# Optimization experiments

Measured on AMD Instinct MI355X. Metric: run time of the kernel, lower is better.

Reference implementation:

```python
import jax, jax.numpy as jnp
import numpy as np

B, S, D = 2, 4096, 768
H = 12
HD = D // H  # 64
INNER = 4 * D
EPS = 1e-5


def setup_inputs() -> dict:
    key = jax.random.key(0)
    ks = jax.random.split(key, 12)
    sd = 0.02
    # causal additive mask (GPT-2 style): 0 where allowed, -1e9 where masked
    causal = jnp.tril(jnp.ones((S, S), dtype=bool))
    attention_mask = jnp.where(causal, 0.0, -1e9).astype(jnp.float32)[None, None]
    return {
        "hidden_states": jax.random.normal(ks[0], (B, S, D), dtype=jnp.float32),
        "attention_mask": attention_mask,
        "ln1_g": jnp.ones((D,), jnp.float32),
        "ln1_b": jnp.zeros((D,), jnp.float32),
        "w_attn": jax.random.normal(ks[1], (D, 3 * D), jnp.float32) * sd,
        "b_attn": jnp.zeros((3 * D,), jnp.float32),
        "w_cproj": jax.random.normal(ks[2], (D, D), jnp.float32) * sd,
        "b_cproj": jnp.zeros((D,), jnp.float32),
        "ln2_g": jnp.ones((D,), jnp.float32),
        "ln2_b": jnp.zeros((D,), jnp.float32),
        "w_fc": jax.random.normal(ks[3], (D, INNER), jnp.float32) * sd,
        "b_fc": jnp.zeros((INNER,), jnp.float32),
        "w_fc_proj": jax.random.normal(ks[4], (INNER, D), jnp.float32) * sd,
        "b_fc_proj": jnp.zeros((D,), jnp.float32),
    }


def _layernorm(x, g, b):
    mu = jnp.mean(x, axis=-1, keepdims=True)
    var = jnp.mean(jnp.square(x - mu), axis=-1, keepdims=True)
    return (x - mu) * jax.lax.rsqrt(var + EPS) * g + b


def reference(hidden_states, attention_mask, ln1_g, ln1_b, w_attn, b_attn,
              w_cproj, b_cproj, ln2_g, ln2_b, w_fc, b_fc, w_fc_proj, b_fc_proj):
    residual = hidden_states
    x = _layernorm(hidden_states, ln1_g, ln1_b)
    # qkv projection
    qkv = x @ w_attn + b_attn                       # [B,S,3D]
    q, k, v = jnp.split(qkv, 3, axis=-1)
    q = q.reshape(B, S, H, HD).transpose(0, 2, 1, 3)  # [B,H,S,HD]
    k = k.reshape(B, S, H, HD).transpose(0, 2, 1, 3)
    v = v.reshape(B, S, H, HD).transpose(0, 2, 1, 3)
    scale = HD ** -0.5
    scores = jnp.einsum('bhqd,bhkd->bhqk', q, k) * scale + attention_mask
    attn = jax.nn.softmax(scores, axis=-1)
    ctx = jnp.einsum('bhqk,bhkd->bhqd', attn, v)    # [B,H,S,HD]
    ctx = ctx.transpose(0, 2, 1, 3).reshape(B, S, D)
    attn_out = ctx @ w_cproj + b_cproj
    h = attn_out + residual
    residual = h
    y = _layernorm(h, ln2_g, ln2_b)
    y = jax.nn.gelu(y @ w_fc + b_fc, approximate=False)  # nn.GELU default = exact
    y = y @ w_fc_proj + b_fc_proj
    return y + residual
```

## Files before the change

kernel.cpp:

```cpp
#include <hip/hip_runtime.h>
#include <hip/hip_bf16.h>


#define S_     4096
#define D_     768
#define H_     12
#define HD_    64
#define NB_    2
#define M_     (NB_*S_)
#define QKV_   (3*D_)
#define INNER_ 3072

typedef unsigned short u16;
typedef __attribute__((ext_vector_type(4))) float f32x4;
typedef __attribute__((ext_vector_type(8))) short s16x8;

__device__ __forceinline__ float bf2f(u16 h) {
    union { unsigned int u; float f; } c; c.u = ((unsigned int)h) << 16; return c.f;
}
__device__ __forceinline__ u16 f2bf(float f) {
    union { float f; unsigned int u; } c; c.f = f;
    return (u16)((c.u + 0x7fffu + ((c.u >> 16) & 1u)) >> 16);
}
__device__ __forceinline__ void storev(u16* p, float v) { *p = f2bf(v); }
__device__ __forceinline__ void storev(float* p, float v) { *p = v; }

__device__ __forceinline__ float fexp2(float x) {
#if __has_builtin(__builtin_amdgcn_exp2f)
    return __builtin_amdgcn_exp2f(x);
#else
    return __expf(x * 0.69314718056f);
#endif
}
__device__ __forceinline__ unsigned int packbf(float a, float b) {
    union { __hip_bfloat162 h; unsigned int u; } c;
    c.h = __float22bfloat162_rn(float2{a, b});
    return c.u;
}

__device__ __forceinline__ void gload_lds16(const u16* g, u16* l) {
    __builtin_amdgcn_global_load_lds((const __attribute__((address_space(1))) void*)g,
                                     (__attribute__((address_space(3))) void*)l, 16, 0, 0);
}

template <typename IT, bool PERM>
__global__ __launch_bounds__(256) void transpose_kernel(const IT* __restrict__ in,
                                                        u16* __restrict__ out,
                                                        int ld_in, int ld_out) {
    __shared__ u16 tile[32][33];
    const int c0 = blockIdx.x * 32, r0 = blockIdx.y * 32;
    const int tx = threadIdx.x & 31, ty = threadIdx.x >> 5;
#pragma unroll
    for (int i = 0; i < 32; i += 8) {
        IT v = in[(size_t)(r0 + ty + i) * ld_in + c0 + tx];
        u16 bv;
        if constexpr (sizeof(IT) == 4) bv = f2bf((float)v); else bv = (u16)v;
        tile[ty + i][tx] = bv;
    }
    __syncthreads();
    int oc = r0 + tx;
    if constexpr (PERM) oc = (oc & ~63) | (((oc & 15) << 2) | ((oc >> 4) & 3));
#pragma unroll
    for (int i = 0; i < 32; i += 8)
        out[(size_t)(c0 + ty + i) * ld_out + oc] = tile[tx][ty + i];
}

__global__ __launch_bounds__(256) void ln_row(const float* __restrict__ x, const float* __restrict__ g,
                                              const float* __restrict__ bb, u16* __restrict__ y) {
    const int row = blockIdx.x;
    const int tid = threadIdx.x;
    const float* xr = x + (size_t)row * D_;
    float v0 = xr[tid], v1 = xr[tid + 256], v2 = xr[tid + 512];
    float s = v0 + v1 + v2, s2 = v0 * v0 + v1 * v1 + v2 * v2;
#pragma unroll
    for (int d = 32; d >= 1; d >>= 1) { s += __shfl_xor(s, d, 64); s2 += __shfl_xor(s2, d, 64); }
    __shared__ float red[8];
    const int wave = tid >> 6, lane = tid & 63;
    if (lane == 0) { red[wave] = s; red[4 + wave] = s2; }
    __syncthreads();
    s = red[0] + red[1] + red[2] + red[3];
    s2 = red[4] + red[5] + red[6] + red[7];
    const float mu = s * (1.0f / D_);
    const float var = s2 * (1.0f / D_) - mu * mu;
    const float rstd = rsqrtf(var + 1e-5f);
    u16* yr = y + (size_t)row * D_;
    yr[tid]       = f2bf((v0 - mu) * rstd * g[tid]       + bb[tid]);
    yr[tid + 256] = f2bf((v1 - mu) * rstd * g[tid + 256] + bb[tid + 256]);
    yr[tid + 512] = f2bf((v2 - mu) * rstd * g[tid + 512] + bb[tid + 512]);
}

template <int EPI, typename OT>
__global__ __launch_bounds__(256) void gemm_bt(const u16* __restrict__ A, const u16* __restrict__ Bt,
                                               const float* __restrict__ bias, const float* res,
                                               OT* C, int M, int N, int K) {
    __shared__ u16 As[128 * 32];
    __shared__ u16 Bs[128 * 32];
    const int tid = threadIdx.x;
    const int wave = tid >> 6, lane = tid & 63;
    const int m0 = blockIdx.y << 7, n0 = blockIdx.x << 7;
    const int fr = lane & 15, quad = lane >> 4;

    const int srow = wave * 16 + (lane >> 2);
    const int scol = (lane & 3) * 8;
    const u16* ag0 = A + (size_t)(m0 + srow) * K + scol;
    const u16* ag1 = ag0 + (size_t)64 * K;
    const u16* bg0 = Bt + (size_t)(n0 + srow) * K + scol;
    const u16* bg1 = bg0 + (size_t)64 * K;
    u16* al0 = As + wave * 512;
    u16* al1 = As + 2048 + wave * 512;
    u16* bl0 = Bs + wave * 512;
    u16* bl1 = Bs + 2048 + wave * 512;

    const f32x4 fz = {0.f, 0.f, 0.f, 0.f};
    f32x4 acc[4][4];
#pragma unroll
    for (int i = 0; i < 4; i++)
#pragma unroll
        for (int j = 0; j < 4; j++) acc[i][j] = fz;

    const int wm = wave & 1, wn = wave >> 1;
    const u16* a_rd = As + (wm * 64 + fr) * 32 + quad * 8;
    const u16* b_rd = Bs + (wn * 64 + fr) * 32 + quad * 8;

    for (int k0 = 0; k0 < K; k0 += 32) {
        gload_lds16(ag0 + k0, al0);
        gload_lds16(ag1 + k0, al1);
        gload_lds16(bg0 + k0, bl0);
        gload_lds16(bg1 + k0, bl1);
        __syncthreads();
        s16x8 af[4], bfr[4];
#pragma unroll
        for (int t = 0; t < 4; t++) {
            af[t]  = *(const s16x8*)(a_rd + t * 16 * 32);
            bfr[t] = *(const s16x8*)(b_rd + t * 16 * 32);
        }
#pragma unroll
        for (int mt = 0; mt < 4; mt++)
#pragma unroll
            for (int nt = 0; nt < 4; nt++)
                acc[mt][nt] = __builtin_amdgcn_mfma_f32_16x16x32_bf16(af[mt], bfr[nt], acc[mt][nt], 0, 0, 0);
        __syncthreads();
    }

    const int crow0 = m0 + wm * 64 + quad * 4;
    const int ccol0 = n0 + wn * 64 + fr;
#pragma unroll
    for (int nt = 0; nt < 4; nt++) {
        const int col = ccol0 + nt * 16;
        const float bv = bias[col];
#pragma unroll
        for (int mt = 0; mt < 4; mt++) {
#pragma unroll
            for (int r = 0; r < 4; r++) {
                const int row = crow0 + mt * 16 + r;
                float v = acc[mt][nt][r] + bv;
                if constexpr (EPI == 1) v = 0.5f * v * (1.0f + erff(v * 0.70710678118654752f));
                if constexpr (EPI == 2) v += res[(size_t)row * N + col];
                storev(&C[(size_t)row * N + col], v);
            }
        }
    }
}

template <int EPI, typename OT>
__global__ __launch_bounds__(256) void gemm_bt64(const u16* __restrict__ A, const u16* __restrict__ Bt,
                                                 const float* __restrict__ bias, const float* res,
                                                 OT* C, int M, int N, int K) {
    __shared__ u16 As[128 * 32];
    __shared__ u16 Bs[64 * 32];
    const int tid = threadIdx.x;
    const int wave = tid >> 6, lane = tid & 63;
    const int m0 = blockIdx.y << 7, n0 = blockIdx.x << 6;
    const int fr = lane & 15, quad = lane >> 4;

    const int srow = wave * 16 + (lane >> 2);
    const int scol = (lane & 3) * 8;
    const u16* ag0 = A + (size_t)(m0 + srow) * K + scol;
    const u16* ag1 = ag0 + (size_t)64 * K;
    const u16* bg0 = Bt + (size_t)(n0 + srow) * K + scol;
    u16* al0 = As + wave * 512;
    u16* al1 = As + 2048 + wave * 512;
    u16* bl0 = Bs + wave * 512;

    const f32x4 fz = {0.f, 0.f, 0.f, 0.f};
    f32x4 acc[2][4];
#pragma unroll
    for (int i = 0; i < 2; i++)
#pragma unroll
        for (int j = 0; j < 4; j++) acc[i][j] = fz;

    const u16* a_rd = As + (wave * 32 + fr) * 32 + quad * 8;
    const u16* b_rd = Bs + fr * 32 + quad * 8;

    for (int k0 = 0; k0 < K; k0 += 32) {
        gload_lds16(ag0 + k0, al0);
        gload_lds16(ag1 + k0, al1);
        gload_lds16(bg0 + k0, bl0);
        __syncthreads();
        s16x8 af[2], bfr[4];
#pragma unroll
        for (int t = 0; t < 2; t++) af[t] = *(const s16x8*)(a_rd + t * 16 * 32);
#pragma unroll
        for (int t = 0; t < 4; t++) bfr[t] = *(const s16x8*)(b_rd + t * 16 * 32);
#pragma unroll
        for (int mt = 0; mt < 2; mt++)
#pragma unroll
            for (int nt = 0; nt < 4; nt++)
                acc[mt][nt] = __builtin_amdgcn_mfma_f32_16x16x32_bf16(af[mt], bfr[nt], acc[mt][nt], 0, 0, 0);
        __syncthreads();
    }

    const int crow0 = m0 + wave * 32 + quad * 4;
    const int ccol0 = n0 + fr;
#pragma unroll
    for (int nt = 0; nt < 4; nt++) {
        const int col = ccol0 + nt * 16;
        const float bv = bias[col];
#pragma unroll
        for (int mt = 0; mt < 2; mt++) {
#pragma unroll
            for (int r = 0; r < 4; r++) {
                const int row = crow0 + mt * 16 + r;
                float v = acc[mt][nt][r] + bv;
                if constexpr (EPI == 1) v = 0.5f * v * (1.0f + erff(v * 0.70710678118654752f));
                if constexpr (EPI == 2) v += res[(size_t)row * N + col];
                storev(&C[(size_t)row * N + col], v);
            }
        }
    }
}

#define SCALE_ 0.1803368801111f
#define PST_ 72
__global__ __launch_bounds__(256, 2) void flash_attn(const u16* __restrict__ qkv, const u16* __restrict__ vt,
                                                     u16* __restrict__ ctx) {
    const int strip = (int)(gridDim.x - 1 - blockIdx.x);
    const int h = blockIdx.y, b = blockIdx.z;
    const int tid = threadIdx.x;
    const int wave = tid >> 6, lane = tid & 63;
    const int fr = lane & 15, quad = lane >> 4;
    const int q0 = strip << 7;
    const int qwv = q0 + (wave << 5);

    __shared__ u16 Ks[2][64 * 64];
    __shared__ u16 Vs[2][64 * 64];
    __shared__ u16 Ps4[4][32 * PST_];
    u16* Ps = Ps4[wave];

    const u16* Qg  = qkv + ((size_t)b * S_ + qwv) * QKV_ + h * HD_;
    const u16* Kg  = qkv + (size_t)b * S_ * QKV_ + D_ + h * HD_;
    const u16* Vtg = vt + ((size_t)b * D_ + h * HD_) * S_;

    const int rsub = lane >> 3;
    const int schunk = ((lane & 7) ^ rsub) << 3;
    const u16* KgS = Kg + (size_t)((wave << 4) + rsub) * QKV_ + schunk;
    const u16* VgS = Vtg + (size_t)((wave << 4) + rsub) * S_ + schunk;
    u16* KlS0 = &Ks[0][(wave << 4) * 64];
    u16* VlS0 = &Vs[0][(wave << 4) * 64];

    s16x8 qf[2][2];
#pragma unroll
    for (int mt = 0; mt < 2; mt++)
#pragma unroll
        for (int kk = 0; kk < 2; kk++)
            qf[mt][kk] = *(const s16x8*)(Qg + (size_t)(mt * 16 + fr) * QKV_ + kk * 32 + quad * 8);

    const f32x4 fz = {0.f, 0.f, 0.f, 0.f};
    f32x4 o[2][4];
    f32x4 ls[2];
#pragma unroll
    for (int mt = 0; mt < 2; mt++) {
        ls[mt] = fz;
#pragma unroll
        for (int nt = 0; nt < 4; nt++) o[mt][nt] = fz;
    }
    s16x8 ones;
#pragma unroll
    for (int j = 0; j < 8; j++) ones[j] = (short)0x3F80;

    const int ntw = (strip << 1) + 2;

    {
        const u16* kg = KgS;
        const u16* vg = VgS;
        gload_lds16(kg, KlS0);
        gload_lds16(kg + (size_t)8 * QKV_, KlS0 + 512);
        gload_lds16(vg, VlS0);
        gload_lds16(vg + (size_t)8 * S_, VlS0 + 512);
    }
    asm volatile("s_waitcnt vmcnt(0)" ::: "memory");
    __syncthreads();

    int cur = 0;
    for (int t = 0; t < ntw; t++) {
        const int k0 = t << 6;

        if (t + 1 < ntw) {
            const int nb = cur ^ 1;
            const u16* kg = KgS + (size_t)((t + 1) << 6) * QKV_;
            const u16* vg = VgS + ((t + 1) << 6);
            u16* kl = KlS0 + nb * (64 * 64);
            u16* vl = VlS0 + nb * (64 * 64);
            gload_lds16(kg, kl);
            gload_lds16(kg + (size_t)8 * QKV_, kl + 512);
            gload_lds16(vg, vl);
            gload_lds16(vg + (size_t)8 * S_, vl + 512);
        }

        if (k0 <= qwv + 31) {
            const u16* kb = Ks[cur];
            const u16* vb = Vs[cur];

            s16x8 kc[2][4];
#pragma unroll
            for (int kk = 0; kk < 2; kk++)
#pragma unroll
                for (int nt = 0; nt < 4; nt++) {
                    const int row = nt * 16 + fr;
                    const int sl = ((kk * 4 + quad) ^ (fr & 7)) << 3;
                    kc[kk][nt] = *(const s16x8*)(kb + row * 64 + sl);
                }

            f32x4 sc[2][4];
#pragma unroll
            for (int mt = 0; mt < 2; mt++)
#pragma unroll
                for (int nt = 0; nt < 4; nt++) sc[mt][nt] = fz;
#pragma unroll
            for (int kk = 0; kk < 2; kk++)
#pragma unroll
                for (int mt = 0; mt < 2; mt++)
#pragma unroll
                    for (int nt = 0; nt < 4; nt++)
                        sc[mt][nt] = __builtin_amdgcn_mfma_f32_16x16x32_bf16(qf[mt][kk], kc[kk][nt], sc[mt][nt], 0, 0, 0);

            const bool fast = (k0 + 63 <= qwv);
#pragma unroll
            for (int mt = 0; mt < 2; mt++) {
#pragma unroll
                for (int r = 0; r < 4; r++) {
                    float s0 = sc[mt][0][r] * SCALE_;
                    float s1 = sc[mt][1][r] * SCALE_;
                    float s2 = sc[mt][2][r] * SCALE_;
                    float s3 = sc[mt][3][r] * SCALE_;
                    if (!fast) {
                        const int lim = (qwv + mt * 16 + quad * 4 + r) - k0;
                        if (fr      > lim) s0 = -1e30f;
                        if (fr + 16 > lim) s1 = -1e30f;
                        if (fr + 32 > lim) s2 = -1e30f;
                        if (fr + 48 > lim) s3 = -1e30f;
                    }
                    s0 = fexp2(s0); s1 = fexp2(s1); s2 = fexp2(s2); s3 = fexp2(s3);
                    const int prow = mt * 16 + quad * 4 + r;
                    *(uint2*)(Ps + prow * PST_ + fr * 4) = make_uint2(packbf(s0, s1), packbf(s2, s3));
                }
            }

            s16x8 vf[2][4];
#pragma unroll
            for (int kk = 0; kk < 2; kk++)
#pragma unroll
                for (int nt = 0; nt < 4; nt++) {
                    const int row = nt * 16 + fr;
                    const int sl = ((kk * 4 + quad) ^ (fr & 7)) << 3;
                    vf[kk][nt] = *(const s16x8*)(vb + row * 64 + sl);
                }

            s16x8 pf[2][2];
#pragma unroll
            for (int mt = 0; mt < 2; mt++)
#pragma unroll
                for (int kk = 0; kk < 2; kk++)
                    pf[mt][kk] = *(const s16x8*)(Ps + (mt * 16 + fr) * PST_ + kk * 32 + quad * 8);

#pragma unroll
            for (int mt = 0; mt < 2; mt++) {
                ls[mt] = __builtin_amdgcn_mfma_f32_16x16x32_bf16(pf[mt][0], ones, ls[mt], 0, 0, 0);
                ls[mt] = __builtin_amdgcn_mfma_f32_16x16x32_bf16(pf[mt][1], ones, ls[mt], 0, 0, 0);
            }
#pragma unroll
            for (int kk = 0; kk < 2; kk++)
#pragma unroll
                for (int mt = 0; mt < 2; mt++)
#pragma unroll
                    for (int nt = 0; nt < 4; nt++)
                        o[mt][nt] = __builtin_amdgcn_mfma_f32_16x16x32_bf16(pf[mt][kk], vf[kk][nt], o[mt][nt], 0, 0, 0);
        }

        asm volatile("s_waitcnt vmcnt(0)" ::: "memory");
        __syncthreads();
        cur ^= 1;
    }

#pragma unroll
    for (int mt = 0; mt < 2; mt++) {
#pragma unroll
        for (int r = 0; r < 4; r++) {
            const int grow = qwv + mt * 16 + quad * 4 + r;
            const float inv = 1.0f / ls[mt][r];
            u16* crow = ctx + ((size_t)b * S_ + grow) * D_ + h * HD_ + fr;
#pragma unroll
            for (int nt = 0; nt < 4; nt++)
                crow[nt * 16] = f2bf(o[mt][nt][r] * inv);
        }
    }
}

extern "C" void kernel_launch(void* const* d_in, const int* in_sizes, int n_in,
                              void* d_out, int out_size, void* d_ws, size_t ws_size,
                              hipStream_t stream) {
    const float* hid    = (const float*)d_in[0];
    const float* ln1g   = (const float*)d_in[2];
    const float* ln1b   = (const float*)d_in[3];
    const float* w_attn = (const float*)d_in[4];
    const float* b_attn = (const float*)d_in[5];
    const float* w_cp   = (const float*)d_in[6];
    const float* b_cp   = (const float*)d_in[7];
    const float* ln2g   = (const float*)d_in[8];
    const float* ln2b   = (const float*)d_in[9];
    const float* w_fc   = (const float*)d_in[10];
    const float* b_fc   = (const float*)d_in[11];
    const float* w_fp   = (const float*)d_in[12];
    const float* b_fp   = (const float*)d_in[13];
    float* dout = (float*)d_out;

    u16* ws = (u16*)d_ws;
    u16* wTa  = ws; ws += (size_t)QKV_ * D_;
    u16* wTc  = ws; ws += (size_t)D_ * D_;
    u16* wTf  = ws; ws += (size_t)INNER_ * D_;
    u16* wTp  = ws; ws += (size_t)D_ * INNER_;
    u16* xln  = ws; ws += (size_t)M_ * D_;
    u16* qkvb = ws; ws += (size_t)M_ * QKV_;
    u16* vtb  = ws; ws += (size_t)NB_ * D_ * S_;
    u16* ctxb = xln;
    u16* yln  = xln;
    u16* act  = qkvb;

    dim3 blk(256);
    transpose_kernel<float, false><<<dim3(QKV_ / 32, D_ / 32), blk, 0, stream>>>(w_attn, wTa, QKV_, D_);
    transpose_kernel<float, false><<<dim3(D_ / 32, D_ / 32), blk, 0, stream>>>(w_cp, wTc, D_, D_);
    transpose_kernel<float, false><<<dim3(INNER_ / 32, D_ / 32), blk, 0, stream>>>(w_fc, wTf, INNER_, D_);
    transpose_kernel<float, false><<<dim3(D_ / 32, INNER_ / 32), blk, 0, stream>>>(w_fp, wTp, D_, INNER_);

    ln_row<<<M_, blk, 0, stream>>>(hid, ln1g, ln1b, xln);
    gemm_bt<0, u16><<<dim3(QKV_ / 128, M_ / 128), blk, 0, stream>>>(xln, wTa, b_attn, nullptr, qkvb, M_, QKV_, D_);

    transpose_kernel<u16, true><<<dim3(D_ / 32, S_ / 32), blk, 0, stream>>>(qkvb + 2 * D_, vtb, QKV_, S_);
    transpose_kernel<u16, true><<<dim3(D_ / 32, S_ / 32), blk, 0, stream>>>(qkvb + (size_t)S_ * QKV_ + 2 * D_,
                                                                            vtb + (size_t)D_ * S_, QKV_, S_);
    flash_attn<<<dim3(S_ / 128, H_, NB_), dim3(256), 0, stream>>>(qkvb, vtb, ctxb);

    gemm_bt64<2, float><<<dim3(D_ / 64, M_ / 128), blk, 0, stream>>>(ctxb, wTc, b_cp, hid, dout, M_, D_, D_);
    ln_row<<<M_, blk, 0, stream>>>(dout, ln2g, ln2b, yln);
    gemm_bt<1, u16><<<dim3(INNER_ / 128, M_ / 128), blk, 0, stream>>>(yln, wTf, b_fc, nullptr, act, M_, INNER_, D_);
    gemm_bt64<2, float><<<dim3(D_ / 64, M_ / 128), blk, 0, stream>>>(act, wTp, b_fp, dout, dout, M_, D_, INNER_);
}
```

Measured before the change: 545.2 us.

## Use persistent flash-attention blocks with atomic work queue, longest strips first

Replaces the fixed 3D grid for flash attention with 512 persistent blocks that fetch work items through an atomic counter. Items are ordered longest causal strip first so that load balancing across CUs improves and the tail is reduced. The counter lives in the output buffer and is zeroed by the first layernorm kernel; the output is overwritten later. This adds an atomic and a barrier per item, plus reliance on the output buffer as scratch.

Measured after the change: 527.9 us. 1.03x faster.

```diff
diff --git a/kernel.cpp b/kernel.cpp
--- a/kernel.cpp
+++ b/kernel.cpp
@@ -66,9 +66,11 @@
 }
 
 __global__ __launch_bounds__(256) void ln_row(const float* __restrict__ x, const float* __restrict__ g,
-                                              const float* __restrict__ bb, u16* __restrict__ y) {
+                                              const float* __restrict__ bb, u16* __restrict__ y,
+                                              unsigned int* ctr) {
     const int row = blockIdx.x;
     const int tid = threadIdx.x;
+    if (ctr && row == 0 && tid == 0) *ctr = 0u;
     const float* xr = x + (size_t)row * D_;
     float v0 = xr[tid], v1 = xr[tid + 256], v2 = xr[tid + 512];
     float s = v0 + v1 + v2, s2 = v0 * v0 + v1 * v1 + v2 * v2;
@@ -230,178 +232,187 @@
     }
 }
 
-#define SCALE_ 0.1803368801111f
-#define PST_ 72
+#define SCALE_  0.1803368801111f
+#define PST_    72
+#define NITEMS_ (32 * H_ * NB_)
+#define NWORK_  512
 __global__ __launch_bounds__(256, 2) void flash_attn(const u16* __restrict__ qkv, const u16* __restrict__ vt,
-                                                     u16* __restrict__ ctx) {
-    const int strip = (int)(gridDim.x - 1 - blockIdx.x);
-    const int h = blockIdx.y, b = blockIdx.z;
+                                                     u16* __restrict__ ctx, unsigned int* __restrict__ ctr) {
     const int tid = threadIdx.x;
     const int wave = tid >> 6, lane = tid & 63;
     const int fr = lane & 15, quad = lane >> 4;
-    const int q0 = strip << 7;
-    const int qwv = q0 + (wave << 5);
 
     __shared__ u16 Ks[2][64 * 64];
     __shared__ u16 Vs[2][64 * 64];
     __shared__ u16 Ps4[4][32 * PST_];
+    __shared__ int item_sh;
     u16* Ps = Ps4[wave];
-
-    const u16* Qg  = qkv + ((size_t)b * S_ + qwv) * QKV_ + h * HD_;
-    const u16* Kg  = qkv + (size_t)b * S_ * QKV_ + D_ + h * HD_;
-    const u16* Vtg = vt + ((size_t)b * D_ + h * HD_) * S_;
 
     const int rsub = lane >> 3;
     const int schunk = ((lane & 7) ^ rsub) << 3;
-    const u16* KgS = Kg + (size_t)((wave << 4) + rsub) * QKV_ + schunk;
-    const u16* VgS = Vtg + (size_t)((wave << 4) + rsub) * S_ + schunk;
     u16* KlS0 = &Ks[0][(wave << 4) * 64];
     u16* VlS0 = &Vs[0][(wave << 4) * 64];
 
-    s16x8 qf[2][2];
-#pragma unroll
-    for (int mt = 0; mt < 2; mt++)
-#pragma unroll
-        for (int kk = 0; kk < 2; kk++)
-            qf[mt][kk] = *(const s16x8*)(Qg + (size_t)(mt * 16 + fr) * QKV_ + kk * 32 + quad * 8);
-
     const f32x4 fz = {0.f, 0.f, 0.f, 0.f};
-    f32x4 o[2][4];
-    f32x4 ls[2];
-#pragma unroll
-    for (int mt = 0; mt < 2; mt++) {
-        ls[mt] = fz;
-#pragma unroll
-        for (int nt = 0; nt < 4; nt++) o[mt][nt] = fz;
-    }
     s16x8 ones;
 #pragma unroll
     for (int j = 0; j < 8; j++) ones[j] = (short)0x3F80;
 
-    const int ntw = (strip << 1) + 2;
-
-    {
-        const u16* kg = KgS;
-        const u16* vg = VgS;
-        gload_lds16(kg, KlS0);
-        gload_lds16(kg + (size_t)8 * QKV_, KlS0 + 512);
-        gload_lds16(vg, VlS0);
-        gload_lds16(vg + (size_t)8 * S_, VlS0 + 512);
-    }
-    asm volatile("s_waitcnt vmcnt(0)" ::: "memory");
-    __syncthreads();
-
-    int cur = 0;
-    for (int t = 0; t < ntw; t++) {
-        const int k0 = t << 6;
-
-        if (t + 1 < ntw) {
-            const int nb = cur ^ 1;
-            const u16* kg = KgS + (size_t)((t + 1) << 6) * QKV_;
-            const u16* vg = VgS + ((t + 1) << 6);
-            u16* kl = KlS0 + nb * (64 * 64);
-            u16* vl = VlS0 + nb * (64 * 64);
-            gload_lds16(kg, kl);
-            gload_lds16(kg + (size_t)8 * QKV_, kl + 512);
-            gload_lds16(vg, vl);
-            gload_lds16(vg + (size_t)8 * S_, vl + 512);
-        }
-
-        if (k0 <= qwv + 31) {
-            const u16* kb = Ks[cur];
-            const u16* vb = Vs[cur];
-
-            s16x8 kc[2][4];
+    for (;;) {
+        if (tid == 0) item_sh = (int)atomicAdd(ctr, 1u);
+        __syncthreads();
+        const int item = item_sh;
+        if (item >= NITEMS_) return;
+
+        const int strip = 31 - item / (H_ * NB_);
+        const int hb = item % (H_ * NB_);
+        const int h = hb % H_, b = hb / H_;
+        const int q0 = strip << 7;
+        const int qwv = q0 + (wave << 5);
+
+        const u16* Qg  = qkv + ((size_t)b * S_ + qwv) * QKV_ + h * HD_;
+        const u16* Kg  = qkv + (size_t)b * S_ * QKV_ + D_ + h * HD_;
+        const u16* Vtg = vt + ((size_t)b * D_ + h * HD_) * S_;
+        const u16* KgS = Kg + (size_t)((wave << 4) + rsub) * QKV_ + schunk;
+        const u16* VgS = Vtg + (size_t)((wave << 4) + rsub) * S_ + schunk;
+
+        s16x8 qf[2][2];
+#pragma unroll
+        for (int mt = 0; mt < 2; mt++)
 #pragma unroll
             for (int kk = 0; kk < 2; kk++)
-#pragma unroll
-                for (int nt = 0; nt < 4; nt++) {
-                    const int row = nt * 16 + fr;
-                    const int sl = ((kk * 4 + quad) ^ (fr & 7)) << 3;
-                    kc[kk][nt] = *(const s16x8*)(kb + row * 64 + sl);
+                qf[mt][kk] = *(const s16x8*)(Qg + (size_t)(mt * 16 + fr) * QKV_ + kk * 32 + quad * 8);
+
+        f32x4 o[2][4];
+        f32x4 ls[2];
+#pragma unroll
+        for (int mt = 0; mt < 2; mt++) {
+            ls[mt] = fz;
+#pragma unroll
+            for (int nt = 0; nt < 4; nt++) o[mt][nt] = fz;
+        }
+
+        const int ntw = (strip << 1) + 2;
+
+        gload_lds16(KgS, KlS0);
+        gload_lds16(KgS + (size_t)8 * QKV_, KlS0 + 512);
+        gload_lds16(VgS, VlS0);
+        gload_lds16(VgS + (size_t)8 * S_, VlS0 + 512);
+        asm volatile("s_waitcnt vmcnt(0)" ::: "memory");
+        __syncthreads();
+
+        int cur = 0;
+        for (int t = 0; t < ntw; t++) {
+            const int k0 = t << 6;
+
+            if (t + 1 < ntw) {
+                const int nb = cur ^ 1;
+                const u16* kg = KgS + (size_t)((t + 1) << 6) * QKV_;
+                const u16* vg = VgS + ((t + 1) << 6);
+                u16* kl = KlS0 + nb * (64 * 64);
+                u16* vl = VlS0 + nb * (64 * 64);
+                gload_lds16(kg, kl);
+                gload_lds16(kg + (size_t)8 * QKV_, kl + 512);
+                gload_lds16(vg, vl);
+                gload_lds16(vg + (size_t)8 * S_, vl + 512);
+            }
+
+            if (k0 <= qwv + 31) {
+                const u16* kb = Ks[cur];
+                const u16* vb = Vs[cur];
+
+                s16x8 kc[2][4];
+#pragma unroll
+                for (int kk = 0; kk < 2; kk++)
+#pragma unroll
+                    for (int nt = 0; nt < 4; nt++) {
+                        const int row = nt * 16 + fr;
+                        const int sl = ((kk * 4 + quad) ^ (fr & 7)) << 3;
+                        kc[kk][nt] = *(const s16x8*)(kb + row * 64 + sl);
+                    }
+
+                f32x4 sc[2][4];
+#pragma unroll
+                for (int mt = 0; mt < 2; mt++)
+#pragma unroll
+                    for (int nt = 0; nt < 4; nt++) sc[mt][nt] = fz;
+#pragma unroll
+                for (int kk = 0; kk < 2; kk++)
+#pragma unroll
+                    for (int mt = 0; mt < 2; mt++)
+#pragma unroll
+                        for (int nt = 0; nt < 4; nt++)
+                            sc[mt][nt] = __builtin_amdgcn_mfma_f32_16x16x32_bf16(qf[mt][kk], kc[kk][nt], sc[mt][nt], 0, 0, 0);
+
+                const bool fast = (k0 + 63 <= qwv);
+#pragma unroll
+                for (int mt = 0; mt < 2; mt++) {
+#pragma unroll
+                    for (int r = 0; r < 4; r++) {
+                        float s0 = sc[mt][0][r] * SCALE_;
+                        float s1 = sc[mt][1][r] * SCALE_;
+                        float s2 = sc[mt][2][r] * SCALE_;
+                        float s3 = sc[mt][3][r] * SCALE_;
+                        if (!fast) {
+                            const int lim = (qwv + mt * 16 + quad * 4 + r) - k0;
+                            if (fr      > lim) s0 = -1e30f;
+                            if (fr + 16 > lim) s1 = -1e30f;
+                            if (fr + 32 > lim) s2 = -1e30f;
+                            if (fr + 48 > lim) s3 = -1e30f;
+                        }
+                        s0 = fexp2(s0); s1 = fexp2(s1); s2 = fexp2(s2); s3 = fexp2(s3);
+                        const int prow = mt * 16 + quad * 4 + r;
+                        *(uint2*)(Ps + prow * PST_ + fr * 4) = make_uint2(packbf(s0, s1), packbf(s2, s3));
+                    }
                 }
 
-            f32x4 sc[2][4];
-#pragma unroll
-            for (int mt = 0; mt < 2; mt++)
-#pragma unroll
-                for (int nt = 0; nt < 4; nt++) sc[mt][nt] = fz;
-#pragma unroll
-            for (int kk = 0; kk < 2; kk++)
+                s16x8 vf[2][4];
+#pragma unroll
+                for (int kk = 0; kk < 2; kk++)
+#pragma unroll
+                    for (int nt = 0; nt < 4; nt++) {
+                        const int row = nt * 16 + fr;
+                        const int sl = ((kk * 4 + quad) ^ (fr & 7)) << 3;
+                        vf[kk][nt] = *(const s16x8*)(vb + row * 64 + sl);
+                    }
+
+                s16x8 pf[2][2];
 #pragma unroll
                 for (int mt = 0; mt < 2; mt++)
 #pragma unroll
-                    for (int nt = 0; nt < 4; nt++)
-                        sc[mt][nt] = __builtin_amdgcn_mfma_f32_16x16x32_bf16(qf[mt][kk], kc[kk][nt], sc[mt][nt], 0, 0, 0);
-
-            const bool fast = (k0 + 63 <= qwv);
-#pragma unroll
-            for (int mt = 0; mt < 2; mt++) {
-#pragma unroll
-                for (int r = 0; r < 4; r++) {
-                    float s0 = sc[mt][0][r] * SCALE_;
-                    float s1 = sc[mt][1][r] * SCALE_;
-                    float s2 = sc[mt][2][r] * SCALE_;
-                    float s3 = sc[mt][3][r] * SCALE_;
-                    if (!fast) {
-                        const int lim = (qwv + mt * 16 + quad * 4 + r) - k0;
-                        if (fr      > lim) s0 = -1e30f;
-                        if (fr + 16 > lim) s1 = -1e30f;
-                        if (fr + 32 > lim) s2 = -1e30f;
-                        if (fr + 48 > lim) s3 = -1e30f;
-                    }
-                    s0 = fexp2(s0); s1 = fexp2(s1); s2 = fexp2(s2); s3 = fexp2(s3);
-                    const int prow = mt * 16 + quad * 4 + r;
-                    *(uint2*)(Ps + prow * PST_ + fr * 4) = make_uint2(packbf(s0, s1), packbf(s2, s3));
+                    for (int kk = 0; kk < 2; kk++)
+                        pf[mt][kk] = *(const s16x8*)(Ps + (mt * 16 + fr) * PST_ + kk * 32 + quad * 8);
+
+#pragma unroll
+                for (int mt = 0; mt < 2; mt++) {
+                    ls[mt] = __builtin_amdgcn_mfma_f32_16x16x32_bf16(pf[mt][0], ones, ls[mt], 0, 0, 0);
+                    ls[mt] = __builtin_amdgcn_mfma_f32_16x16x32_bf16(pf[mt][1], ones, ls[mt], 0, 0, 0);
                 }
+#pragma unroll
+                for (int kk = 0; kk < 2; kk++)
+#pragma unroll
+                    for (int mt = 0; mt < 2; mt++)
+#pragma unroll
+                        for (int nt = 0; nt < 4; nt++)
+                            o[mt][nt] = __builtin_amdgcn_mfma_f32_16x16x32_bf16(pf[mt][kk], vf[kk][nt], o[mt][nt], 0, 0, 0);
             }
 
-            s16x8 vf[2][4];
-#pragma unroll
-            for (int kk = 0; kk < 2; kk++)
-#pragma unroll
-                for (int nt = 0; nt < 4; nt++) {
-                    const int row = nt * 16 + fr;
-                    const int sl = ((kk * 4 + quad) ^ (fr & 7)) << 3;
-                    vf[kk][nt] = *(const s16x8*)(vb + row * 64 + sl);
-                }
-
-            s16x8 pf[2][2];
-#pragma unroll
-            for (int mt = 0; mt < 2; mt++)
-#pragma unroll
-                for (int kk = 0; kk < 2; kk++)
-                    pf[mt][kk] = *(const s16x8*)(Ps + (mt * 16 + fr) * PST_ + kk * 32 + quad * 8);
-
-#pragma unroll
-            for (int mt = 0; mt < 2; mt++) {
-                ls[mt] = __builtin_amdgcn_mfma_f32_16x16x32_bf16(pf[mt][0], ones, ls[mt], 0, 0, 0);
-                ls[mt] = __builtin_amdgcn_mfma_f32_16x16x32_bf16(pf[mt][1], ones, ls[mt], 0, 0, 0);
+            asm volatile("s_waitcnt vmcnt(0)" ::: "memory");
+            __syncthreads();
+            cur ^= 1;
+        }
+
+#pragma unroll
+        for (int mt = 0; mt < 2; mt++) {
+#pragma unroll
+            for (int r = 0; r < 4; r++) {
+                const int grow = qwv + mt * 16 + quad * 4 + r;
+                const float inv = 1.0f / ls[mt][r];
+                u16* crow = ctx + ((size_t)b * S_ + grow) * D_ + h * HD_ + fr;
+#pragma unroll
+                for (int nt = 0; nt < 4; nt++)
+                    crow[nt * 16] = f2bf(o[mt][nt][r] * inv);
             }
-#pragma unroll
-            for (int kk = 0; kk < 2; kk++)
-#pragma unroll
-                for (int mt = 0; mt < 2; mt++)
-#pragma unroll
-                    for (int nt = 0; nt < 4; nt++)
-                        o[mt][nt] = __builtin_amdgcn_mfma_f32_16x16x32_bf16(pf[mt][kk], vf[kk][nt], o[mt][nt], 0, 0, 0);
-        }
-
-        asm volatile("s_waitcnt vmcnt(0)" ::: "memory");
-        __syncthreads();
-        cur ^= 1;
-    }
-
-#pragma unroll
-    for (int mt = 0; mt < 2; mt++) {
-#pragma unroll
-        for (int r = 0; r < 4; r++) {
-            const int grow = qwv + mt * 16 + quad * 4 + r;
-            const float inv = 1.0f / ls[mt][r];
-            u16* crow = ctx + ((size_t)b * S_ + grow) * D_ + h * HD_ + fr;
-#pragma unroll
-            for (int nt = 0; nt < 4; nt++)
-                crow[nt * 16] = f2bf(o[mt][nt][r] * inv);
         }
     }
 }
@@ -424,6 +435,8 @@
     const float* b_fp   = (const float*)d_in[13];
     float* dout = (float*)d_out;
 
+    unsigned int* ctr = (unsigned int*)d_out;
+
     u16* ws = (u16*)d_ws;
     u16* wTa  = ws; ws += (size_t)QKV_ * D_;
     u16* wTc  = ws; ws += (size_t)D_ * D_;
@@ -442,16 +455,16 @@
     transpose_kernel<float, false><<<dim3(INNER_ / 32, D_ / 32), blk, 0, stream>>>(w_fc, wTf, INNER_, D_);
     transpose_kernel<float, false><<<dim3(D_ / 32, INNER_ / 32), blk, 0, stream>>>(w_fp, wTp, D_, INNER_);
 
-    ln_row<<<M_, blk, 0, stream>>>(hid, ln1g, ln1b, xln);
+    ln_row<<<M_, blk, 0, stream>>>(hid, ln1g, ln1b, xln, ctr);
     gemm_bt<0, u16><<<dim3(QKV_ / 128, M_ / 128), blk, 0, stream>>>(xln, wTa, b_attn, nullptr, qkvb, M_, QKV_, D_);
 
     transpose_kernel<u16, true><<<dim3(D_ / 32, S_ / 32), blk, 0, stream>>>(qkvb + 2 * D_, vtb, QKV_, S_);
     transpose_kernel<u16, true><<<dim3(D_ / 32, S_ / 32), blk, 0, stream>>>(qkvb + (size_t)S_ * QKV_ + 2 * D_,
                                                                             vtb + (size_t)D_ * S_, QKV_, S_);
-    flash_attn<<<dim3(S_ / 128, H_, NB_), dim3(256), 0, stream>>>(qkvb, vtb, ctxb);
+    flash_attn<<<dim3(NWORK_), blk, 0, stream>>>(qkvb, vtb, ctxb, ctr);
 
     gemm_bt64<2, float><<<dim3(D_ / 64, M_ / 128), blk, 0, stream>>>(ctxb, wTc, b_cp, hid, dout, M_, D_, D_);
-    ln_row<<<M_, blk, 0, stream>>>(dout, ln2g, ln2b, yln);
+    ln_row<<<M_, blk, 0, stream>>>(dout, ln2g, ln2b, yln, nullptr);
     gemm_bt<1, u16><<<dim3(INNER_ / 128, M_ / 128), blk, 0, stream>>>(yln, wTf, b_fc, nullptr, act, M_, INNER_, D_);
     gemm_bt64<2, float><<<dim3(D_ / 64, M_ / 128), blk, 0, stream>>>(act, wTp, b_fp, dout, dout, M_, D_, INNER_);
 }
```
